# Optimization experiments

Measured on AMD Instinct MI355X. Metric: run time of the kernel, lower is better.

The kernel has to match this reference:

```python
import jax, jax.numpy as jnp
import numpy as np

N = [32768, 8192, 2048, 512, 128]  # mesh sizes per level
SEQ = 9
B = 16
LATENT = 256


def spiral_conv(x, idx, W, b):
    # x: (B, N_in, C); idx: (Nn, SEQ) -> (B, Nn, out)
    Bn, Nn = x.shape[0], idx.shape[0]
    g = x[:, idx.reshape(-1), :].reshape(Bn, Nn, -1)  # gather spiral neighborhoods
    return g @ W.T + b


def pool(x, row, col, val, n_out):
    # sparse transform: out[b, row] += x[b, col] * val  (index_select * value -> scatter_add)
    y = x[:, col, :] * val[None, :, None]
    return jnp.zeros((x.shape[0], n_out, x.shape[-1]), x.dtype).at[:, row, :].add(y)


def setup_inputs() -> dict:
    key = jax.random.key(0)
    ks = iter(jax.random.split(key, 96))
    d = {}
    d["x"] = jax.random.normal(next(ks), (B, N[0], 3), jnp.float32)
    for i in range(4):
        d[f"si{i}"] = jax.random.randint(next(ks), (N[i], SEQ), 0, N[i], dtype=jnp.int32)
    for i in range(4):
        d[f"d{i}_row"] = jnp.repeat(jnp.arange(N[i + 1], dtype=jnp.int32), 3)
        d[f"d{i}_col"] = jax.random.randint(next(ks), (3 * N[i + 1],), 0, N[i], dtype=jnp.int32)
        d[f"d{i}_val"] = jax.random.uniform(next(ks), (3 * N[i + 1],), jnp.float32)
        d[f"u{i}_row"] = jnp.repeat(jnp.arange(N[i], dtype=jnp.int32), 3)
        d[f"u{i}_col"] = jax.random.randint(next(ks), (3 * N[i],), 0, N[i + 1], dtype=jnp.int32)
        d[f"u{i}_val"] = jax.random.uniform(next(ks), (3 * N[i],), jnp.float32)
    def w(k, shape):
        return jax.random.normal(k, shape, jnp.float32) * 0.05
    enc_in = [3, 32, 32, 32]
    enc_out = [32, 32, 32, 64]
    for i in range(4):
        d[f"enW{i}"] = w(next(ks), (enc_out[i], enc_in[i] * SEQ))
        d[f"enb{i}"] = jnp.zeros((enc_out[i],), jnp.float32)
    d["fcW"] = w(next(ks), (LATENT, N[4] * 64))
    d["fcb"] = jnp.zeros((LATENT,), jnp.float32)
    d["dfcW"] = w(next(ks), (N[4] * 64, LATENT))
    d["dfcb"] = jnp.zeros((N[4] * 64,), jnp.float32)
    dec_in = [64, 64, 32, 32]
    dec_out = [64, 32, 32, 32]
    for i in range(4):
        d[f"deW{i}"] = w(next(ks), (dec_out[i], dec_in[i] * SEQ))
        d[f"deb{i}"] = jnp.zeros((dec_out[i],), jnp.float32)
    d["outW"] = w(next(ks), (3, 32 * SEQ))
    d["outb"] = jnp.zeros((3,), jnp.float32)
    return d


def reference(x, si0, si1, si2, si3,
              d0_row, d0_col, d0_val, d1_row, d1_col, d1_val,
              d2_row, d2_col, d2_val, d3_row, d3_col, d3_val,
              u0_row, u0_col, u0_val, u1_row, u1_col, u1_val,
              u2_row, u2_col, u2_val, u3_row, u3_col, u3_val,
              enW0, enb0, enW1, enb1, enW2, enb2, enW3, enb3,
              fcW, fcb, dfcW, dfcb,
              deW0, deb0, deW1, deb1, deW2, deb2, deW3, deb3,
              outW, outb):
    si = [si0, si1, si2, si3]
    dn = [(d0_row, d0_col, d0_val), (d1_row, d1_col, d1_val), (d2_row, d2_col, d2_val), (d3_row, d3_col, d3_val)]
    up = [(u0_row, u0_col, u0_val), (u1_row, u1_col, u1_val), (u2_row, u2_col, u2_val), (u3_row, u3_col, u3_val)]
    enW = [enW0, enW1, enW2, enW3]
    enb = [enb0, enb1, enb2, enb3]
    deW = [deW0, deW1, deW2, deW3]
    deb = [deb0, deb1, deb2, deb3]
    # encoder: SpiralEnblock = elu(spiral_conv) -> down pool
    h = x
    for i in range(4):
        h = jax.nn.elu(spiral_conv(h, si[i], enW[i], enb[i]))
        h = pool(h, dn[i][0], dn[i][1], dn[i][2], N[i + 1])
    h = h.reshape(h.shape[0], -1)  # (B, N4*64)
    mu = jax.nn.sigmoid(h @ fcW.T + fcb)  # non-VAE branch: sigmoid, logvar=None
    z = mu
    # decoder
    h = (z @ dfcW.T + dfcb).reshape(-1, N[4], 64)
    for i in range(4):  # SpiralDeblock = up pool -> elu(spiral_conv)
        lvl = 3 - i
        h = pool(h, up[lvl][0], up[lvl][1], up[lvl][2], N[lvl])
        h = jax.nn.elu(spiral_conv(h, si[lvl], deW[i], deb[i]))
    out = spiral_conv(h, si[0], outW, outb)
    return (out, z, mu)
```

## Files before the change

### kernel.cpp

```cpp
#include <hip/hip_runtime.h>
#include <cstdint>
#include <cstddef>

#define BATCH 16

static constexpr int NN0 = 32768, NN1 = 8192, NN2 = 2048, NN3 = 512, NN4 = 128;

__device__ __forceinline__ float fast_elu(float a) {
    return a > 0.f ? a : __expf(a) - 1.f;
}

struct TD { const float* W; float* Wt; int CO, K, off; };
struct TA { TD d[8]; int total; };

__global__ __launch_bounds__(256) void transpose_all(TA a) {
    int i = blockIdx.x * 256 + threadIdx.x;
    if (i >= a.total) return;
    #pragma unroll
    for (int j = 0; j < 8; ++j) {
        const TD t = a.d[j];
        if (i >= t.off && i < t.off + t.CO * t.K) {
            int e = i - t.off, c = e / t.K, k = e - c * t.K;
            t.Wt[k * t.CO + c] = t.W[e];
            return;
        }
    }
}

__global__ __launch_bounds__(256) void conv0_v4(const float* __restrict__ x,
                                                const int* __restrict__ idx,
                                                const float* __restrict__ Wt,
                                                const float* __restrict__ bias,
                                                float* __restrict__ out,
                                                int N) {
    const int v = blockIdx.x * 256 + threadIdx.x;
    const int b = blockIdx.y;
    const float* __restrict__ xb = x + (size_t)b * N * 3;

    int nb[9];
    #pragma unroll
    for (int s = 0; s < 9; ++s) nb[s] = idx[(size_t)v * 9 + s];

    float g[27];
    #pragma unroll
    for (int s = 0; s < 9; ++s) {
        const float* __restrict__ p = xb + (size_t)nb[s] * 3;
        g[s * 3 + 0] = p[0]; g[s * 3 + 1] = p[1]; g[s * 3 + 2] = p[2];
    }

    float acc[32];
    #pragma unroll
    for (int c = 0; c < 32; ++c) acc[c] = bias[c];

    #pragma unroll
    for (int k = 0; k < 27; ++k) {
        const float gk = g[k];
        const float* __restrict__ wr = Wt + k * 32;
        #pragma unroll
        for (int c = 0; c < 32; ++c) acc[c] += gk * wr[c];
    }

    float* __restrict__ o = out + ((size_t)b * N + v) * 32;
    #pragma unroll
    for (int q = 0; q < 8; ++q) {
        float4 t;
        t.x = fast_elu(acc[q * 4 + 0]);
        t.y = fast_elu(acc[q * 4 + 1]);
        t.z = fast_elu(acc[q * 4 + 2]);
        t.w = fast_elu(acc[q * 4 + 3]);
        *reinterpret_cast<float4*>(o + q * 4) = t;
    }
}

template<int CIN, int COUT, bool ELU>
__global__ __launch_bounds__(256) void conv_v3(const float* __restrict__ x,
                                               const int* __restrict__ idx,
                                               const float* __restrict__ Wt,
                                               const float* __restrict__ bias,
                                               float* __restrict__ out,
                                               int N) {
    static_assert(COUT % 16 == 0, "COUT multiple of 16");
    constexpr int QG    = COUT / 16;
    static_assert(QG <= 4 && 4 % QG == 0, "QG in {1,2,4}");
    constexpr int VSETS = 4 / QG;
    constexpr int VPB   = 64 * VSETS;
    constexpr int GS    = CIN + 4;
    constexpr int CQ    = CIN / 4;

    __shared__ float g[VPB][GS];
    __shared__ int   nbr[VPB][9];

    const int b  = blockIdx.y;
    const int v0 = blockIdx.x * VPB;
    const float* __restrict__ xb = x + (size_t)b * N * CIN;

    for (int t = threadIdx.x; t < VPB * 9; t += 256)
        nbr[t / 9][t % 9] = idx[(size_t)v0 * 9 + t];

    const int wv   = __builtin_amdgcn_readfirstlane(threadIdx.x >> 6);
    const int lane = threadIdx.x & 63;
    const int vset = wv / QG;
    const int qg   = wv % QG;
    const int vloc = vset * 64 + lane;

    float4 acc[4];
    #pragma unroll
    for (int q = 0; q < 4; ++q) acc[q] = make_float4(0.f, 0.f, 0.f, 0.f);

    for (int s = 0; s < 9; ++s) {
        __syncthreads();
        constexpr int GSLOTS = VPB * CQ;
        static_assert(GSLOTS % 256 == 0, "staging divisibility");
        #pragma unroll
        for (int p = 0; p < GSLOTS / 256; ++p) {
            const int slot = p * 256 + threadIdx.x;
            const int v = slot / CQ, q = slot - v * CQ;
            const float4 t4 = *reinterpret_cast<const float4*>(
                xb + (size_t)nbr[v][s] * CIN + q * 4);
            *reinterpret_cast<float4*>(&g[v][q * 4]) = t4;
        }
        __syncthreads();

        const float* __restrict__ wbase = Wt + (size_t)s * CIN * COUT + qg * 16;
        #pragma unroll
        for (int k4 = 0; k4 < CQ; ++k4) {
            const float4 gv = *reinterpret_cast<const float4*>(&g[vloc][k4 * 4]);
            #pragma unroll
            for (int kk = 0; kk < 4; ++kk) {
                const float* __restrict__ wr = wbase + (size_t)(k4 * 4 + kk) * COUT;
                const float4 w0 = *reinterpret_cast<const float4*>(wr);
                const float4 w1 = *reinterpret_cast<const float4*>(wr + 4);
                const float4 w2 = *reinterpret_cast<const float4*>(wr + 8);
                const float4 w3 = *reinterpret_cast<const float4*>(wr + 12);
                const float gk = (kk == 0) ? gv.x : (kk == 1) ? gv.y : (kk == 2) ? gv.z : gv.w;
                acc[0].x += gk * w0.x; acc[0].y += gk * w0.y; acc[0].z += gk * w0.z; acc[0].w += gk * w0.w;
                acc[1].x += gk * w1.x; acc[1].y += gk * w1.y; acc[1].z += gk * w1.z; acc[1].w += gk * w1.w;
                acc[2].x += gk * w2.x; acc[2].y += gk * w2.y; acc[2].z += gk * w2.z; acc[2].w += gk * w2.w;
                acc[3].x += gk * w3.x; acc[3].y += gk * w3.y; acc[3].z += gk * w3.z; acc[3].w += gk * w3.w;
            }
        }
    }

    float* __restrict__ orow = out + ((size_t)b * N + v0 + vloc) * COUT + qg * 16;
    #pragma unroll
    for (int q = 0; q < 4; ++q) {
        const float4 bv = *reinterpret_cast<const float4*>(bias + qg * 16 + q * 4);
        float4 a = acc[q];
        a.x += bv.x; a.y += bv.y; a.z += bv.z; a.w += bv.w;
        if constexpr (ELU) {
            a.x = fast_elu(a.x);
            a.y = fast_elu(a.y);
            a.z = fast_elu(a.z);
            a.w = fast_elu(a.w);
        }
        *reinterpret_cast<float4*>(orow + q * 4) = a;
    }
}

__global__ __launch_bounds__(256) void out_conv_v3(const float* __restrict__ x,
                                                   const int* __restrict__ idx,
                                                   const float* __restrict__ W,
                                                   const float* __restrict__ bias,
                                                   float* __restrict__ out,
                                                   int N) {
    constexpr int VPB = 256;
    constexpr int GS  = 36;
    __shared__ float g[VPB][GS];
    __shared__ int   nbr[VPB][9];

    const int b  = blockIdx.y;
    const int v0 = blockIdx.x * VPB;
    const float* __restrict__ xb = x + (size_t)b * N * 32;

    for (int t = threadIdx.x; t < VPB * 9; t += 256)
        nbr[t / 9][t % 9] = idx[(size_t)v0 * 9 + t];

    const int vloc = threadIdx.x;
    float a0 = 0.f, a1 = 0.f, a2 = 0.f;

    for (int s = 0; s < 9; ++s) {
        __syncthreads();
        #pragma unroll
        for (int p = 0; p < 8; ++p) {
            const int slot = p * 256 + threadIdx.x;
            const int v = slot / 8, q = slot - v * 8;
            const float4 t4 = *reinterpret_cast<const float4*>(
                xb + (size_t)nbr[v][s] * 32 + q * 4);
            *reinterpret_cast<float4*>(&g[v][q * 4]) = t4;
        }
        __syncthreads();
        #pragma unroll
        for (int k4 = 0; k4 < 8; ++k4) {
            const float4 gv = *reinterpret_cast<const float4*>(&g[vloc][k4 * 4]);
            const float4 w0 = *reinterpret_cast<const float4*>(W +   0 + s * 32 + k4 * 4);
            const float4 w1 = *reinterpret_cast<const float4*>(W + 288 + s * 32 + k4 * 4);
            const float4 w2 = *reinterpret_cast<const float4*>(W + 576 + s * 32 + k4 * 4);
            a0 += gv.x * w0.x + gv.y * w0.y + gv.z * w0.z + gv.w * w0.w;
            a1 += gv.x * w1.x + gv.y * w1.y + gv.z * w1.z + gv.w * w1.w;
            a2 += gv.x * w2.x + gv.y * w2.y + gv.z * w2.z + gv.w * w2.w;
        }
    }

    float* o = out + ((size_t)b * N + v0 + vloc) * 3;
    o[0] = a0 + bias[0]; o[1] = a1 + bias[1]; o[2] = a2 + bias[2];
}

template<int C>
__global__ __launch_bounds__(256) void pool_kernel(const float* __restrict__ x,
                                                   const int* __restrict__ col,
                                                   const float* __restrict__ val,
                                                   float* __restrict__ out,
                                                   int Nout, int Nin) {
    constexpr int CQ = C / 4;
    const int q = blockIdx.x * 256 + threadIdx.x;
    if (q >= BATCH * Nout * CQ) return;
    const int cq = q % CQ;
    const int r  = (q / CQ) % Nout;
    const int b  = q / (CQ * Nout);
    float ax = 0.f, ay = 0.f, az = 0.f, aw = 0.f;
    #pragma unroll
    for (int j = 0; j < 3; ++j) {
        const int   c0 = col[3 * r + j];
        const float vl = val[3 * r + j];
        const float4 xv = *reinterpret_cast<const float4*>(
            x + ((size_t)b * Nin + c0) * C + cq * 4);
        ax += vl * xv.x; ay += vl * xv.y; az += vl * xv.z; aw += vl * xv.w;
    }
    float4 o; o.x = ax; o.y = ay; o.z = az; o.w = aw;
    *reinterpret_cast<float4*>(out + ((size_t)b * Nout + r) * C + cq * 4) = o;
}

__global__ __launch_bounds__(256) void fc_enc_kernel(const float* __restrict__ h,
                                                     const float* __restrict__ W,
                                                     const float* __restrict__ bias,
                                                     float* __restrict__ z,
                                                     float* __restrict__ out_z,
                                                     float* __restrict__ out_mu) {
    const int l = blockIdx.x;
    const float* __restrict__ wr = W + (size_t)l * 8192;
    float acc[BATCH];
    #pragma unroll
    for (int b = 0; b < BATCH; ++b) acc[b] = 0.f;
    for (int k = threadIdx.x * 4; k < 8192; k += 256 * 4) {
        const float4 w4 = *reinterpret_cast<const float4*>(wr + k);
        #pragma unroll
        for (int b = 0; b < BATCH; ++b) {
            const float4 h4 = *reinterpret_cast<const float4*>(h + (size_t)b * 8192 + k);
            acc[b] += w4.x * h4.x + w4.y * h4.y + w4.z * h4.z + w4.w * h4.w;
        }
    }
    __shared__ float red[BATCH][4];
    const int wid = threadIdx.x >> 6, lane = threadIdx.x & 63;
    #pragma unroll
    for (int b = 0; b < BATCH; ++b) {
        float v = acc[b];
        for (int off = 32; off; off >>= 1) v += __shfl_down(v, off);
        if (lane == 0) red[b][wid] = v;
    }
    __syncthreads();
    if (threadIdx.x < BATCH) {
        const int b = threadIdx.x;
        float s = red[b][0] + red[b][1] + red[b][2] + red[b][3] + bias[l];
        s = 1.f / (1.f + expf(-s));
        z[b * 256 + l]      = s;
        out_z[b * 256 + l]  = s;
        out_mu[b * 256 + l] = s;
    }
}

__global__ __launch_bounds__(256) void fc_dec_kernel(const float* __restrict__ z,
                                                     const float* __restrict__ W,
                                                     const float* __restrict__ bias,
                                                     float* __restrict__ out) {
    __shared__ float zl[BATCH * 256];
    for (int t = threadIdx.x; t < BATCH * 256; t += 256) zl[t] = z[t];
    __syncthreads();
    const int m = blockIdx.x * 256 + threadIdx.x;
    const float* __restrict__ wr = W + (size_t)m * 256;
    float acc[BATCH];
    #pragma unroll
    for (int b = 0; b < BATCH; ++b) acc[b] = 0.f;
    for (int l = 0; l < 256; l += 4) {
        const float4 w4 = *reinterpret_cast<const float4*>(wr + l);
        #pragma unroll
        for (int b = 0; b < BATCH; ++b) {
            acc[b] += w4.x * zl[b * 256 + l]     + w4.y * zl[b * 256 + l + 1]
                    + w4.z * zl[b * 256 + l + 2] + w4.w * zl[b * 256 + l + 3];
        }
    }
    const float bm = bias[m];
    #pragma unroll
    for (int b = 0; b < BATCH; ++b) out[(size_t)b * 8192 + m] = acc[b] + bm;
}

extern "C" void kernel_launch(void* const* d_in, const int* in_sizes, int n_in,
                              void* d_out, int out_size, void* d_ws, size_t ws_size,
                              hipStream_t stream) {
    (void)in_sizes; (void)n_in; (void)out_size; (void)ws_size;

    const float* x = (const float*)d_in[0];
    const int* si[4] = {(const int*)d_in[1], (const int*)d_in[2],
                        (const int*)d_in[3], (const int*)d_in[4]};
    const int*   dcol[4]; const float* dval[4];
    const int*   ucol[4]; const float* uval[4];
    for (int i = 0; i < 4; ++i) {
        dcol[i] = (const int*)  d_in[5 + 6 * i + 1];
        dval[i] = (const float*)d_in[5 + 6 * i + 2];
        ucol[i] = (const int*)  d_in[5 + 6 * i + 4];
        uval[i] = (const float*)d_in[5 + 6 * i + 5];
    }
    const float *enW[4], *enb[4], *deW[4], *deb[4];
    for (int i = 0; i < 4; ++i) {
        enW[i] = (const float*)d_in[29 + 2 * i];
        enb[i] = (const float*)d_in[30 + 2 * i];
        deW[i] = (const float*)d_in[41 + 2 * i];
        deb[i] = (const float*)d_in[42 + 2 * i];
    }
    const float* fcW  = (const float*)d_in[37];
    const float* fcb  = (const float*)d_in[38];
    const float* dfcW = (const float*)d_in[39];
    const float* dfcb = (const float*)d_in[40];
    const float* outW = (const float*)d_in[49];
    const float* outb = (const float*)d_in[50];

    float* ws = (float*)d_ws;
    float* A  = ws;
    float* Bb = A  + (size_t)BATCH * NN0 * 32;
    float* z  = Bb + (size_t)BATCH * NN0 * 32;
    float* wt_en0 = z + BATCH * 256;
    float* wt_en1 = wt_en0 + 27  * 32;
    float* wt_en2 = wt_en1 + 288 * 32;
    float* wt_en3 = wt_en2 + 288 * 32;
    float* wt_de0 = wt_en3 + 288 * 64;
    float* wt_de1 = wt_de0 + 576 * 64;
    float* wt_de2 = wt_de1 + 576 * 32;
    float* wt_de3 = wt_de2 + 288 * 32;

    float* out    = (float*)d_out;
    float* out_z  = out + (size_t)BATCH * NN0 * 3;
    float* out_mu = out_z + BATCH * 256;

    {
        TA ta; int off = 0;
        auto add = [&](int j, const float* W, float* Wt, int CO, int K) {
            ta.d[j] = TD{W, Wt, CO, K, off}; off += CO * K;
        };
        add(0, enW[0], wt_en0, 32, 27);
        add(1, enW[1], wt_en1, 32, 288);
        add(2, enW[2], wt_en2, 32, 288);
        add(3, enW[3], wt_en3, 64, 288);
        add(4, deW[0], wt_de0, 64, 576);
        add(5, deW[1], wt_de1, 32, 576);
        add(6, deW[2], wt_de2, 32, 288);
        add(7, deW[3], wt_de3, 32, 288);
        ta.total = off;
        transpose_all<<<(off + 255) / 256, 256, 0, stream>>>(ta);
    }

    conv0_v4<<<dim3(NN0 / 256, BATCH), 256, 0, stream>>>(x, si[0], wt_en0, enb[0], A, NN0);
    pool_kernel<32><<<(BATCH * NN1 * 8) / 256, 256, 0, stream>>>(A, dcol[0], dval[0], Bb, NN1, NN0);
    conv_v3<32, 32, true><<<dim3(NN1 / 128, BATCH), 256, 0, stream>>>(Bb, si[1], wt_en1, enb[1], A, NN1);
    pool_kernel<32><<<(BATCH * NN2 * 8) / 256, 256, 0, stream>>>(A, dcol[1], dval[1], Bb, NN2, NN1);
    conv_v3<32, 32, true><<<dim3(NN2 / 128, BATCH), 256, 0, stream>>>(Bb, si[2], wt_en2, enb[2], A, NN2);
    pool_kernel<32><<<(BATCH * NN3 * 8) / 256, 256, 0, stream>>>(A, dcol[2], dval[2], Bb, NN3, NN2);
    conv_v3<32, 64, true><<<dim3(NN3 / 64, BATCH), 256, 0, stream>>>(Bb, si[3], wt_en3, enb[3], A, NN3);
    pool_kernel<64><<<(BATCH * NN4 * 16) / 256, 256, 0, stream>>>(A, dcol[3], dval[3], Bb, NN4, NN3);

    fc_enc_kernel<<<256, 256, 0, stream>>>(Bb, fcW, fcb, z, out_z, out_mu);
    fc_dec_kernel<<<32, 256, 0, stream>>>(z, dfcW, dfcb, A);

    pool_kernel<64><<<(BATCH * NN3 * 16) / 256, 256, 0, stream>>>(A, ucol[3], uval[3], Bb, NN3, NN4);
    conv_v3<64, 64, true><<<dim3(NN3 / 64, BATCH), 256, 0, stream>>>(Bb, si[3], wt_de0, deb[0], A, NN3);
    pool_kernel<64><<<(BATCH * NN2 * 16) / 256, 256, 0, stream>>>(A, ucol[2], uval[2], Bb, NN2, NN3);
    conv_v3<64, 32, true><<<dim3(NN2 / 128, BATCH), 256, 0, stream>>>(Bb, si[2], wt_de1, deb[1], A, NN2);
    pool_kernel<32><<<(BATCH * NN1 * 8) / 256, 256, 0, stream>>>(A, ucol[1], uval[1], Bb, NN1, NN2);
    conv_v3<32, 32, true><<<dim3(NN1 / 128, BATCH), 256, 0, stream>>>(Bb, si[1], wt_de2, deb[2], A, NN1);
    pool_kernel<32><<<(BATCH * NN0 * 8) / 256, 256, 0, stream>>>(A, ucol[0], uval[0], Bb, NN0, NN1);
    conv_v3<32, 32, true><<<dim3(NN0 / 128, BATCH), 256, 0, stream>>>(Bb, si[0], wt_de3, deb[3], A, NN0);

    out_conv_v3<<<dim3(NN0 / 256, BATCH), 256, 0, stream>>>(A, si[0], outW, outb, out, NN0);
}
```

Measured before the change: 753.8 us.

## Swizzle block order so each XCD owns one batch, and prefetch gathered rows

All conv and pool kernels now use a 1D grid whose block ids are decoded so that every block on a given XCD (id & 7) works on the same one or two batch items. Each XCD's L2 then holds that batch's activations, which improves locality for the random neighbour gathers. The conv kernel also loads the next spiral step's gathered rows into registers while computing the current step, so global gathers overlap the FMA work. The output conv drops LDS staging in favour of direct per-thread gathers with a tighter launch bound. The swizzle relies on the block-to-XCD round-robin assumption and on a batch of exactly 16, and the register prefetch raises register pressure.

```diff
diff --git a/kernel.cpp b/kernel.cpp
--- a/kernel.cpp
+++ b/kernel.cpp
@@ -27,58 +27,21 @@
     }
 }
 
-__global__ __launch_bounds__(256) void conv0_v4(const float* __restrict__ x,
-                                                const int* __restrict__ idx,
-                                                const float* __restrict__ Wt,
-                                                const float* __restrict__ bias,
-                                                float* __restrict__ out,
-                                                int N) {
-    const int v = blockIdx.x * 256 + threadIdx.x;
-    const int b = blockIdx.y;
-    const float* __restrict__ xb = x + (size_t)b * N * 3;
-
-    int nb[9];
-    #pragma unroll
-    for (int s = 0; s < 9; ++s) nb[s] = idx[(size_t)v * 9 + s];
-
-    float g[27];
-    #pragma unroll
-    for (int s = 0; s < 9; ++s) {
-        const float* __restrict__ p = xb + (size_t)nb[s] * 3;
-        g[s * 3 + 0] = p[0]; g[s * 3 + 1] = p[1]; g[s * 3 + 2] = p[2];
-    }
-
-    float acc[32];
-    #pragma unroll
-    for (int c = 0; c < 32; ++c) acc[c] = bias[c];
-
-    #pragma unroll
-    for (int k = 0; k < 27; ++k) {
-        const float gk = g[k];
-        const float* __restrict__ wr = Wt + k * 32;
-        #pragma unroll
-        for (int c = 0; c < 32; ++c) acc[c] += gk * wr[c];
-    }
-
-    float* __restrict__ o = out + ((size_t)b * N + v) * 32;
-    #pragma unroll
-    for (int q = 0; q < 8; ++q) {
-        float4 t;
-        t.x = fast_elu(acc[q * 4 + 0]);
-        t.y = fast_elu(acc[q * 4 + 1]);
-        t.z = fast_elu(acc[q * 4 + 2]);
-        t.w = fast_elu(acc[q * 4 + 3]);
-        *reinterpret_cast<float4*>(o + q * 4) = t;
-    }
+__device__ __forceinline__ void swz_decode(int id, int GX, int& bx, int& b) {
+    const int xcd = id & 7;
+    const int j   = id >> 3;
+    const int hf  = (j >= GX) ? 1 : 0;
+    bx = j - (hf ? GX : 0);
+    b  = xcd + 8 * hf;
 }
 
 template<int CIN, int COUT, bool ELU>
-__global__ __launch_bounds__(256) void conv_v3(const float* __restrict__ x,
+__global__ __launch_bounds__(256) void conv_v5(const float* __restrict__ x,
                                                const int* __restrict__ idx,
                                                const float* __restrict__ Wt,
                                                const float* __restrict__ bias,
                                                float* __restrict__ out,
-                                               int N) {
+                                               int N, int GX) {
     static_assert(COUT % 16 == 0, "COUT multiple of 16");
     constexpr int QG    = COUT / 16;
     static_assert(QG <= 4 && 4 % QG == 0, "QG in {1,2,4}");
@@ -86,16 +49,20 @@
     constexpr int VPB   = 64 * VSETS;
     constexpr int GS    = CIN + 4;
     constexpr int CQ    = CIN / 4;
+    constexpr int GP    = (VPB * CQ) / 256;
+    static_assert((VPB * CQ) % 256 == 0, "staging divisibility");
 
     __shared__ float g[VPB][GS];
     __shared__ int   nbr[VPB][9];
 
-    const int b  = blockIdx.y;
-    const int v0 = blockIdx.x * VPB;
+    int bx, b;
+    swz_decode(blockIdx.x, GX, bx, b);
+    const int v0 = bx * VPB;
     const float* __restrict__ xb = x + (size_t)b * N * CIN;
 
     for (int t = threadIdx.x; t < VPB * 9; t += 256)
         nbr[t / 9][t % 9] = idx[(size_t)v0 * 9 + t];
+    __syncthreads();
 
     const int wv   = __builtin_amdgcn_readfirstlane(threadIdx.x >> 6);
     const int lane = threadIdx.x & 63;
@@ -103,24 +70,35 @@
     const int qg   = wv % QG;
     const int vloc = vset * 64 + lane;
 
-    float4 acc[4];
-    #pragma unroll
-    for (int q = 0; q < 4; ++q) acc[q] = make_float4(0.f, 0.f, 0.f, 0.f);
-
-    for (int s = 0; s < 9; ++s) {
-        __syncthreads();
-        constexpr int GSLOTS = VPB * CQ;
-        static_assert(GSLOTS % 256 == 0, "staging divisibility");
-        #pragma unroll
-        for (int p = 0; p < GSLOTS / 256; ++p) {
+    float4 r[GP];
+    auto issue_loads = [&](int s) {
+        #pragma unroll
+        for (int p = 0; p < GP; ++p) {
             const int slot = p * 256 + threadIdx.x;
             const int v = slot / CQ, q = slot - v * CQ;
-            const float4 t4 = *reinterpret_cast<const float4*>(
+            r[p] = *reinterpret_cast<const float4*>(
                 xb + (size_t)nbr[v][s] * CIN + q * 4);
-            *reinterpret_cast<float4*>(&g[v][q * 4]) = t4;
-        }
-        __syncthreads();
-
+        }
+    };
+    auto write_lds = [&]() {
+        #pragma unroll
+        for (int p = 0; p < GP; ++p) {
+            const int slot = p * 256 + threadIdx.x;
+            const int v = slot / CQ, q = slot - v * CQ;
+            *reinterpret_cast<float4*>(&g[v][q * 4]) = r[p];
+        }
+    };
+
+    float4 acc[4];
+    #pragma unroll
+    for (int q = 0; q < 4; ++q) acc[q] = make_float4(0.f, 0.f, 0.f, 0.f);
+
+    issue_loads(0);
+    write_lds();
+    __syncthreads();
+
+    for (int s = 0; s < 9; ++s) {
+        if (s < 8) issue_loads(s + 1);
         const float* __restrict__ wbase = Wt + (size_t)s * CIN * COUT + qg * 16;
         #pragma unroll
         for (int k4 = 0; k4 < CQ; ++k4) {
@@ -139,6 +117,8 @@
                 acc[3].x += gk * w3.x; acc[3].y += gk * w3.y; acc[3].z += gk * w3.z; acc[3].w += gk * w3.w;
             }
         }
+        __syncthreads();
+        if (s < 8) { write_lds(); __syncthreads(); }
     }
 
     float* __restrict__ orow = out + ((size_t)b * N + v0 + vloc) * COUT + qg * 16;
@@ -148,75 +128,112 @@
         float4 a = acc[q];
         a.x += bv.x; a.y += bv.y; a.z += bv.z; a.w += bv.w;
         if constexpr (ELU) {
-            a.x = fast_elu(a.x);
-            a.y = fast_elu(a.y);
-            a.z = fast_elu(a.z);
-            a.w = fast_elu(a.w);
+            a.x = fast_elu(a.x); a.y = fast_elu(a.y);
+            a.z = fast_elu(a.z); a.w = fast_elu(a.w);
         }
         *reinterpret_cast<float4*>(orow + q * 4) = a;
     }
 }
 
-__global__ __launch_bounds__(256) void out_conv_v3(const float* __restrict__ x,
-                                                   const int* __restrict__ idx,
-                                                   const float* __restrict__ W,
-                                                   const float* __restrict__ bias,
-                                                   float* __restrict__ out,
-                                                   int N) {
-    constexpr int VPB = 256;
-    constexpr int GS  = 36;
-    __shared__ float g[VPB][GS];
-    __shared__ int   nbr[VPB][9];
-
-    const int b  = blockIdx.y;
-    const int v0 = blockIdx.x * VPB;
+__global__ __launch_bounds__(256) void conv0_v5(const float* __restrict__ x,
+                                                const int* __restrict__ idx,
+                                                const float* __restrict__ Wt,
+                                                const float* __restrict__ bias,
+                                                float* __restrict__ out,
+                                                int N, int GX) {
+    int bx, b;
+    swz_decode(blockIdx.x, GX, bx, b);
+    const int v = bx * 256 + threadIdx.x;
+    const float* __restrict__ xb = x + (size_t)b * N * 3;
+
+    int nb[9];
+    #pragma unroll
+    for (int s = 0; s < 9; ++s) nb[s] = idx[(size_t)v * 9 + s];
+
+    float g[27];
+    #pragma unroll
+    for (int s = 0; s < 9; ++s) {
+        const float* __restrict__ p = xb + (size_t)nb[s] * 3;
+        g[s * 3 + 0] = p[0]; g[s * 3 + 1] = p[1]; g[s * 3 + 2] = p[2];
+    }
+
+    float acc[32];
+    #pragma unroll
+    for (int c = 0; c < 32; ++c) acc[c] = bias[c];
+
+    #pragma unroll
+    for (int k = 0; k < 27; ++k) {
+        const float gk = g[k];
+        const float* __restrict__ wr = Wt + k * 32;
+        #pragma unroll
+        for (int c = 0; c < 32; ++c) acc[c] += gk * wr[c];
+    }
+
+    float* __restrict__ o = out + ((size_t)b * N + v) * 32;
+    #pragma unroll
+    for (int q = 0; q < 8; ++q) {
+        float4 t;
+        t.x = fast_elu(acc[q * 4 + 0]);
+        t.y = fast_elu(acc[q * 4 + 1]);
+        t.z = fast_elu(acc[q * 4 + 2]);
+        t.w = fast_elu(acc[q * 4 + 3]);
+        *reinterpret_cast<float4*>(o + q * 4) = t;
+    }
+}
+
+__global__ __launch_bounds__(256, 4) void out_conv_v4(const float* __restrict__ x,
+                                                      const int* __restrict__ idx,
+                                                      const float* __restrict__ W,
+                                                      const float* __restrict__ bias,
+                                                      float* __restrict__ out,
+                                                      int N, int GX) {
+    int bx, b;
+    swz_decode(blockIdx.x, GX, bx, b);
+    const int v = bx * 256 + threadIdx.x;
     const float* __restrict__ xb = x + (size_t)b * N * 32;
 
-    for (int t = threadIdx.x; t < VPB * 9; t += 256)
-        nbr[t / 9][t % 9] = idx[(size_t)v0 * 9 + t];
-
-    const int vloc = threadIdx.x;
+    int nb[9];
+    #pragma unroll
+    for (int s = 0; s < 9; ++s) nb[s] = idx[(size_t)v * 9 + s];
+
     float a0 = 0.f, a1 = 0.f, a2 = 0.f;
-
+    #pragma unroll
     for (int s = 0; s < 9; ++s) {
-        __syncthreads();
-        #pragma unroll
-        for (int p = 0; p < 8; ++p) {
-            const int slot = p * 256 + threadIdx.x;
-            const int v = slot / 8, q = slot - v * 8;
-            const float4 t4 = *reinterpret_cast<const float4*>(
-                xb + (size_t)nbr[v][s] * 32 + q * 4);
-            *reinterpret_cast<float4*>(&g[v][q * 4]) = t4;
-        }
-        __syncthreads();
-        #pragma unroll
-        for (int k4 = 0; k4 < 8; ++k4) {
-            const float4 gv = *reinterpret_cast<const float4*>(&g[vloc][k4 * 4]);
-            const float4 w0 = *reinterpret_cast<const float4*>(W +   0 + s * 32 + k4 * 4);
-            const float4 w1 = *reinterpret_cast<const float4*>(W + 288 + s * 32 + k4 * 4);
-            const float4 w2 = *reinterpret_cast<const float4*>(W + 576 + s * 32 + k4 * 4);
-            a0 += gv.x * w0.x + gv.y * w0.y + gv.z * w0.z + gv.w * w0.w;
-            a1 += gv.x * w1.x + gv.y * w1.y + gv.z * w1.z + gv.w * w1.w;
-            a2 += gv.x * w2.x + gv.y * w2.y + gv.z * w2.z + gv.w * w2.w;
-        }
-    }
-
-    float* o = out + ((size_t)b * N + v0 + vloc) * 3;
+        const float* __restrict__ xs = xb + (size_t)nb[s] * 32;
+        #pragma unroll
+        for (int q = 0; q < 8; ++q) {
+            const float4 xv = *reinterpret_cast<const float4*>(xs + q * 4);
+            const float4 w0 = *reinterpret_cast<const float4*>(W +   0 + s * 32 + q * 4);
+            const float4 w1 = *reinterpret_cast<const float4*>(W + 288 + s * 32 + q * 4);
+            const float4 w2 = *reinterpret_cast<const float4*>(W + 576 + s * 32 + q * 4);
+            a0 += xv.x * w0.x + xv.y * w0.y + xv.z * w0.z + xv.w * w0.w;
+            a1 += xv.x * w1.x + xv.y * w1.y + xv.z * w1.z + xv.w * w1.w;
+            a2 += xv.x * w2.x + xv.y * w2.y + xv.z * w2.z + xv.w * w2.w;
+        }
+    }
+
+    float* __restrict__ o = out + ((size_t)b * N + v) * 3;
     o[0] = a0 + bias[0]; o[1] = a1 + bias[1]; o[2] = a2 + bias[2];
 }
 
 template<int C>
-__global__ __launch_bounds__(256) void pool_kernel(const float* __restrict__ x,
-                                                   const int* __restrict__ col,
-                                                   const float* __restrict__ val,
-                                                   float* __restrict__ out,
-                                                   int Nout, int Nin) {
+__global__ __launch_bounds__(256) void pool_v2(const float* __restrict__ x,
+                                               const int* __restrict__ col,
+                                               const float* __restrict__ val,
+                                               float* __restrict__ out,
+                                               int Nout, int Nin, int bpb) {
     constexpr int CQ = C / 4;
-    const int q = blockIdx.x * 256 + threadIdx.x;
-    if (q >= BATCH * Nout * CQ) return;
-    const int cq = q % CQ;
-    const int r  = (q / CQ) % Nout;
-    const int b  = q / (CQ * Nout);
+    const int id  = blockIdx.x;
+    const int xcd = id & 7;
+    const int jj  = id >> 3;
+    const int hf  = (jj >= bpb) ? 1 : 0;
+    const int inner = jj - (hf ? bpb : 0);
+    const int b   = xcd + 8 * hf;
+
+    const int t  = inner * 256 + threadIdx.x;
+    const int cq = t % CQ;
+    const int r  = t / CQ;
+
     float ax = 0.f, ay = 0.f, az = 0.f, aw = 0.f;
     #pragma unroll
     for (int j = 0; j < 3; ++j) {
@@ -357,26 +374,37 @@
         transpose_all<<<(off + 255) / 256, 256, 0, stream>>>(ta);
     }
 
-    conv0_v4<<<dim3(NN0 / 256, BATCH), 256, 0, stream>>>(x, si[0], wt_en0, enb[0], A, NN0);
-    pool_kernel<32><<<(BATCH * NN1 * 8) / 256, 256, 0, stream>>>(A, dcol[0], dval[0], Bb, NN1, NN0);
-    conv_v3<32, 32, true><<<dim3(NN1 / 128, BATCH), 256, 0, stream>>>(Bb, si[1], wt_en1, enb[1], A, NN1);
-    pool_kernel<32><<<(BATCH * NN2 * 8) / 256, 256, 0, stream>>>(A, dcol[1], dval[1], Bb, NN2, NN1);
-    conv_v3<32, 32, true><<<dim3(NN2 / 128, BATCH), 256, 0, stream>>>(Bb, si[2], wt_en2, enb[2], A, NN2);
-    pool_kernel<32><<<(BATCH * NN3 * 8) / 256, 256, 0, stream>>>(A, dcol[2], dval[2], Bb, NN3, NN2);
-    conv_v3<32, 64, true><<<dim3(NN3 / 64, BATCH), 256, 0, stream>>>(Bb, si[3], wt_en3, enb[3], A, NN3);
-    pool_kernel<64><<<(BATCH * NN4 * 16) / 256, 256, 0, stream>>>(A, dcol[3], dval[3], Bb, NN4, NN3);
+    auto pool32 = [&](const float* in, const int* col, const float* val,
+                      float* o, int Nout, int Nin) {
+        const int bpb = Nout * 8 / 256;
+        pool_v2<32><<<bpb * BATCH, 256, 0, stream>>>(in, col, val, o, Nout, Nin, bpb);
+    };
+    auto pool64 = [&](const float* in, const int* col, const float* val,
+                      float* o, int Nout, int Nin) {
+        const int bpb = Nout * 16 / 256;
+        pool_v2<64><<<bpb * BATCH, 256, 0, stream>>>(in, col, val, o, Nout, Nin, bpb);
+    };
+
+    conv0_v5<<<(NN0 / 256) * BATCH, 256, 0, stream>>>(x, si[0], wt_en0, enb[0], A, NN0, NN0 / 256);
+    pool32(A, dcol[0], dval[0], Bb, NN1, NN0);
+    conv_v5<32, 32, true><<<(NN1 / 128) * BATCH, 256, 0, stream>>>(Bb, si[1], wt_en1, enb[1], A, NN1, NN1 / 128);
+    pool32(A, dcol[1], dval[1], Bb, NN2, NN1);
+    conv_v5<32, 32, true><<<(NN2 / 128) * BATCH, 256, 0, stream>>>(Bb, si[2], wt_en2, enb[2], A, NN2, NN2 / 128);
+    pool32(A, dcol[2], dval[2], Bb, NN3, NN2);
+    conv_v5<32, 64, true><<<(NN3 / 64) * BATCH, 256, 0, stream>>>(Bb, si[3], wt_en3, enb[3], A, NN3, NN3 / 64);
+    pool64(A, dcol[3], dval[3], Bb, NN4, NN3);
 
     fc_enc_kernel<<<256, 256, 0, stream>>>(Bb, fcW, fcb, z, out_z, out_mu);
     fc_dec_kernel<<<32, 256, 0, stream>>>(z, dfcW, dfcb, A);
 
-    pool_kernel<64><<<(BATCH * NN3 * 16) / 256, 256, 0, stream>>>(A, ucol[3], uval[3], Bb, NN3, NN4);
-    conv_v3<64, 64, true><<<dim3(NN3 / 64, BATCH), 256, 0, stream>>>(Bb, si[3], wt_de0, deb[0], A, NN3);
-    pool_kernel<64><<<(BATCH * NN2 * 16) / 256, 256, 0, stream>>>(A, ucol[2], uval[2], Bb, NN2, NN3);
-    conv_v3<64, 32, true><<<dim3(NN2 / 128, BATCH), 256, 0, stream>>>(Bb, si[2], wt_de1, deb[1], A, NN2);
-    pool_kernel<32><<<(BATCH * NN1 * 8) / 256, 256, 0, stream>>>(A, ucol[1], uval[1], Bb, NN1, NN2);
-    conv_v3<32, 32, true><<<dim3(NN1 / 128, BATCH), 256, 0, stream>>>(Bb, si[1], wt_de2, deb[2], A, NN1);
-    pool_kernel<32><<<(BATCH * NN0 * 8) / 256, 256, 0, stream>>>(A, ucol[0], uval[0], Bb, NN0, NN1);
-    conv_v3<32, 32, true><<<dim3(NN0 / 128, BATCH), 256, 0, stream>>>(Bb, si[0], wt_de3, deb[3], A, NN0);
-
-    out_conv_v3<<<dim3(NN0 / 256, BATCH), 256, 0, stream>>>(A, si[0], outW, outb, out, NN0);
-}
+    pool64(A, ucol[3], uval[3], Bb, NN3, NN4);
+    conv_v5<64, 64, true><<<(NN3 / 64) * BATCH, 256, 0, stream>>>(Bb, si[3], wt_de0, deb[0], A, NN3, NN3 / 64);
+    pool64(A, ucol[2], uval[2], Bb, NN2, NN3);
+    conv_v5<64, 32, true><<<(NN2 / 128) * BATCH, 256, 0, stream>>>(Bb, si[2], wt_de1, deb[1], A, NN2, NN2 / 128);
+    pool32(A, ucol[1], uval[1], Bb, NN1, NN2);
+    conv_v5<32, 32, true><<<(NN1 / 128) * BATCH, 256, 0, stream>>>(Bb, si[1], wt_de2, deb[2], A, NN1, NN1 / 128);
+    pool32(A, ucol[0], uval[0], Bb, NN0, NN1);
+    conv_v5<32, 32, true><<<(NN0 / 128) * BATCH, 256, 0, stream>>>(Bb, si[0], wt_de3, deb[3], A, NN0, NN0 / 128);
+
+    out_conv_v4<<<(NN0 / 256) * BATCH, 256, 0, stream>>>(A, si[0], outW, outb, out, NN0, NN0 / 256);
+}
```

After: 1.466 ms. +94.5%, slower.
